# Kernel tuning notes

Measured on AMD Instinct MI355X. Metric: run time of the kernel, lower is better.

## Reference

```python
import jax, jax.numpy as jnp
import numpy as np
from jax import lax

B, T = 32, 512
CHAR_V, WORD_V, K = 120, 100000, 15
E = 128            # char/word embedding dim
D = 2 * E          # fusion dim = 256
H = 128            # hidden per direction (hidden_dim // 2)
L = 2              # num LSTM layers


def setup_inputs() -> dict:
    key = jax.random.key(0)
    ks = jax.random.split(key, 16)
    char_ids = jax.random.randint(ks[0], (B, T), 0, CHAR_V)
    word_ids = jax.random.randint(ks[1], (B, T), 0, WORD_V)
    tags = jax.random.randint(ks[2], (B, T), 0, K)
    mask = jnp.ones((B, T), dtype=bool)
    s = 0.1
    char_emb = jax.random.normal(ks[3], (CHAR_V, E), jnp.float32) * s
    char_emb = char_emb.at[0].set(0.0)  # padding_idx=0
    word_emb = jax.random.normal(ks[4], (WORD_V, E), jnp.float32) * s
    word_emb = word_emb.at[0].set(0.0)
    # Both layers have input dim D (layer0: fusion 256, layer1: bi-output 256),
    # so stack params as (layer, direction, ...). PyTorch gate order: i,f,g,o.
    lstm_wih = jax.random.normal(ks[5], (L, 2, 4 * H, D), jnp.float32) * s
    lstm_whh = jax.random.normal(ks[6], (L, 2, 4 * H, H), jnp.float32) * s
    lstm_bih = jax.random.normal(ks[7], (L, 2, 4 * H), jnp.float32) * s
    lstm_bhh = jax.random.normal(ks[8], (L, 2, 4 * H), jnp.float32) * s
    fc_w = jax.random.normal(ks[9], (K, 2 * H), jnp.float32) * s
    fc_b = jax.random.normal(ks[10], (K,), jnp.float32) * s
    trans = jax.random.normal(ks[11], (K, K), jnp.float32) * s
    start_trans = jax.random.normal(ks[12], (K,), jnp.float32) * s
    end_trans = jax.random.normal(ks[13], (K,), jnp.float32) * s
    return dict(char_ids=char_ids, word_ids=word_ids, tags=tags, mask=mask,
                char_emb=char_emb, word_emb=word_emb,
                lstm_wih=lstm_wih, lstm_whh=lstm_whh,
                lstm_bih=lstm_bih, lstm_bhh=lstm_bhh,
                fc_w=fc_w, fc_b=fc_b,
                trans=trans, start_trans=start_trans, end_trans=end_trans)


def _lstm_dir(xs, wih, whh, bih, bhh, reverse):
    # xs: (T, B, Din) -> hs: (T, B, H)
    pre = jnp.einsum('tbd,hd->tbh', xs, wih) + bih + bhh  # hoisted input GEMM
    h0 = jnp.zeros((xs.shape[1], whh.shape[1]), xs.dtype)
    def step(carry, p):
        h, c = carry
        g = p + h @ whh.T
        i, f, gg, o = jnp.split(g, 4, axis=-1)
        c = jax.nn.sigmoid(f) * c + jax.nn.sigmoid(i) * jnp.tanh(gg)
        h = jax.nn.sigmoid(o) * jnp.tanh(c)
        return (h, c), h
    _, hs = lax.scan(step, (h0, h0), pre, reverse=reverse)
    return hs


def _crf_nll(emissions, tags, maskf, trans, start, end):
    # emissions (T,B,K), tags (T,B) int, maskf (T,B) float. Returns -sum(logL).
    Tn, Bn, Kn = emissions.shape
    bidx = jnp.arange(Bn)
    # numerator: score of gold path
    num0 = start[tags[0]] + emissions[0, bidx, tags[0]]
    def nstep(s, inp):
        em_t, tg_t, tg_p, m_t = inp
        return s + (trans[tg_p, tg_t] + em_t[bidx, tg_t]) * m_t, None
    num, _ = lax.scan(nstep, num0, (emissions[1:], tags[1:], tags[:-1], maskf[1:]))
    seq_ends = maskf.sum(0).astype(jnp.int32) - 1
    num = num + end[tags[seq_ends, bidx]]
    # denominator: forward algorithm (logsumexp over all paths)
    alpha0 = start[None, :] + emissions[0]  # (B,K)
    def dstep(a, inp):
        em_t, m_t = inp
        nxt = jax.nn.logsumexp(a[:, :, None] + trans[None] + em_t[:, None, :], axis=1)
        return jnp.where(m_t[:, None] > 0, nxt, a), None
    alpha, _ = lax.scan(dstep, alpha0, (emissions[1:], maskf[1:]))
    den = jax.nn.logsumexp(alpha + end[None, :], axis=1)
    return -(num - den).sum()


def reference(char_ids, word_ids, tags, mask, char_emb, word_emb,
              lstm_wih, lstm_whh, lstm_bih, lstm_bhh,
              fc_w, fc_b, trans, start_trans, end_trans):
    fused = jnp.concatenate([char_emb[char_ids], word_emb[word_ids]], axis=-1)  # (B,T,256)
    xs = fused.transpose(1, 0, 2)  # (T,B,256)
    for l in range(L):  # dropout is identity in eval/deterministic reference
        hf = _lstm_dir(xs, lstm_wih[l, 0], lstm_whh[l, 0], lstm_bih[l, 0], lstm_bhh[l, 0], False)
        hb = _lstm_dir(xs, lstm_wih[l, 1], lstm_whh[l, 1], lstm_bih[l, 1], lstm_bhh[l, 1], True)
        xs = jnp.concatenate([hf, hb], axis=-1)  # (T,B,256)
    emissions = jnp.einsum('tbh,kh->tbk', xs, fc_w) + fc_b  # (T,B,15)
    maskf = mask.T.astype(emissions.dtype)
    return _crf_nll(emissions, tags.T, maskf, trans, start_trans, end_trans)
```

## Files before the change

kernel.cpp:

```cpp
#include <hip/hip_runtime.h>

#define TT 512
#define BB 32
#define KK 15
#define PGD 8

typedef __attribute__((ext_vector_type(8))) short short8;
typedef __attribute__((ext_vector_type(4))) float f32x4;
typedef __attribute__((ext_vector_type(8))) unsigned short us8;
typedef __attribute__((ext_vector_type(4))) unsigned short us4;
typedef __attribute__((ext_vector_type(2))) unsigned int u32x2;

__device__ __forceinline__ float bf2f(unsigned short u){
  union { unsigned int i; float f; } v; v.i = ((unsigned int)u) << 16; return v.f;
}
__device__ __forceinline__ unsigned short f2bf(float f){
  union { float f; unsigned int i; } v; v.f = f;
  return (unsigned short)((v.i + 0x7fffu + ((v.i >> 16) & 1u)) >> 16);
}
__device__ __forceinline__ float bflo(unsigned int u){ return __int_as_float((int)(u << 16)); }
__device__ __forceinline__ float bfhi(unsigned int u){ return __int_as_float((int)(u & 0xffff0000u)); }

__global__ void k_prep_embed(const float* __restrict__ wih, const float* __restrict__ whh,
                       const float* __restrict__ bih, const float* __restrict__ bhh,
                       const float* __restrict__ fcw,
                       unsigned short* __restrict__ wih_bf, unsigned short* __restrict__ whh_bf,
                       float* __restrict__ bias, unsigned short* __restrict__ fcw_bf,
                       const int* __restrict__ cid, const int* __restrict__ wid,
                       const float* __restrict__ cemb, const float* __restrict__ wemb,
                       unsigned short* __restrict__ x){
  int bx = blockIdx.x, tid = threadIdx.x;
  if (bx < 2048){
    int i = bx * 256 + tid;
    if (i < 2*2*512*256) wih_bf[i] = f2bf(wih[i]);
    if (i < 2*2*512*128) whh_bf[i] = f2bf(whh[i]);
    if (i < 2*2*512)     bias[i]   = bih[i] + bhh[i];
    if (i < 16*256)      fcw_bf[i] = (i < 15*256) ? f2bf(fcw[i]) : (unsigned short)0;
  } else {
    int m = (bx - 2048)*2 + (tid >> 7);
    int d = tid & 127;
    int t = m >> 5, b = m & 31;
    int c = cid[b*TT + t], w = wid[b*TT + t];
    x[(size_t)m*256 + d]       = f2bf(cemb[c*128 + d]);
    x[(size_t)m*256 + 128 + d] = f2bf(wemb[(size_t)w*128 + d]);
  }
}

__global__ __launch_bounds__(256) void k_gemm_pre(const unsigned short* __restrict__ x,
                        const unsigned short* __restrict__ wih_bf,
                        const float* __restrict__ bias,
                        unsigned short* __restrict__ pre){
  int lane = threadIdx.x & 63, wv = threadIdx.x >> 6;
  int m0 = blockIdx.x * 128 + wv * 32;
  int t = m0 >> 5;
  int by = blockIdx.y;
  int r16 = lane & 15, q4 = lane >> 4;
  const unsigned short* arow0 = x + (size_t)(m0 + r16)*256 + q4*8;
  const unsigned short* arow1 = arow0 + 16*256;
  short8 a0[8], a1[8];
  #pragma unroll
  for (int ks = 0; ks < 8; ++ks){ a0[ks] = *(const short8*)(arow0 + ks*32);
                                  a1[ks] = *(const short8*)(arow1 + ks*32); }
  f32x4 acc0[8], acc1[8];
  float bs[8];
  #pragma unroll
  for (int sub = 0; sub < 8; ++sub){
    int dir = sub >> 2, g = sub & 3;
    int n0 = dir*512 + g*128 + by*16;
    const unsigned short* brow = wih_bf + (size_t)(n0 + r16)*256 + q4*8;
    f32x4 z0 = {0.f,0.f,0.f,0.f}, z1 = {0.f,0.f,0.f,0.f};
    #pragma unroll
    for (int ks = 0; ks < 8; ++ks){
      short8 bfr = *(const short8*)(brow + ks*32);
      z0 = __builtin_amdgcn_mfma_f32_16x16x32_bf16(a0[ks], bfr, z0, 0, 0, 0);
      z1 = __builtin_amdgcn_mfma_f32_16x16x32_bf16(a1[ks], bfr, z1, 0, 0, 0);
    }
    acc0[sub] = z0; acc1[sub] = z1;
    bs[sub] = bias[n0 + r16];
  }
  #pragma unroll
  for (int dir = 0; dir < 2; ++dir){
    size_t pb0 = ((((size_t)dir*TT + t)*8 + q4)*8 + by)*256;
    size_t pb1 = ((((size_t)dir*TT + t)*8 + 4 + q4)*8 + by)*256;
    #pragma unroll
    for (int rr = 0; rr < 4; ++rr){
      us4 s0, s1;
      #pragma unroll
      for (int g = 0; g < 4; ++g){
        s0[g] = f2bf(acc0[dir*4+g][rr] + bs[dir*4+g]);
        s1[g] = f2bf(acc1[dir*4+g][rr] + bs[dir*4+g]);
      }
      *(us4*)(pre + pb0 + (size_t)((r16*4 + rr)*4)) = s0;
      *(us4*)(pre + pb1 + (size_t)((r16*4 + rr)*4)) = s1;
    }
  }
}

__global__ __launch_bounds__(512) void k_lstm(const unsigned short* __restrict__ pre,
                                              const unsigned short* __restrict__ whh_bf,
                                              unsigned short* __restrict__ y){
  const int dir = blockIdx.x >> 3, grp = blockIdx.x & 7;
  const int tid = threadIdx.x, lane = tid & 63, w = tid >> 6;
  const int r16 = lane & 15, q4 = lane >> 4;
  __shared__ __align__(16) unsigned char hbuf[2*1024];
  __shared__ __align__(16) unsigned char scratch[8*1024];
  *(unsigned int*)(hbuf + tid*4) = 0u;

  short8 afrag[4][4];
  const unsigned short* whhd = whh_bf + (size_t)dir*512*128;
  #pragma unroll
  for (int j = 0; j < 4; ++j){
    int wrow = (r16 & 3)*128 + w*16 + j*4 + (r16 >> 2);
    #pragma unroll
    for (int ks = 0; ks < 4; ++ks)
      afrag[j][ks] = *(const short8*)(whhd + (size_t)wrow*128 + ks*32 + q4*8);
  }

  const int t0 = dir ? TT-1 : 0;
  const ptrdiff_t ts = dir ? -16384 : 16384;
  const unsigned short* gbase = pre + ((((size_t)dir*TT + t0)*8 + grp)*8 + w)*256 + lane*4;
  u32x2 pgbuf[PGD];
  #pragma unroll
  for (int s = 0; s < PGD; ++s) pgbuf[s] = *(const u32x2*)(gbase + s*ts);
  const unsigned short* gptr = gbase + PGD*ts;

  const unsigned sw = (unsigned)(r16 << 5);
  const unsigned char* hb = hbuf + r16*256;
  const unsigned bo0 = (  0u + q4*16) ^ sw, bo1 = ( 64u + q4*16) ^ sw,
                 bo2 = (128u + q4*16) ^ sw, bo3 = (192u + q4*16) ^ sw;
  const unsigned scw_off = (unsigned)(size_t)(__attribute__((address_space(3))) unsigned char*)
                           (scratch + w*1024 + q4*32 + r16*8);
  const unsigned char* scr8 = scratch + w*1024 + (size_t)lane*8;
  const int hc = w*16 + (lane >> 2), bbn = lane & 3;
  unsigned char* hwp = hbuf + bbn*256 + (((unsigned)(hc*2)) ^ (bbn << 5));
  const bool act4 = (r16 < 4);
  const bool yw = (w < 4) && act4;
  const ptrdiff_t tsy = dir ? -(BB*256) : (BB*256);
  unsigned short* ysptr = y + ((size_t)t0*BB + grp*4 + r16)*256 + dir*128 + w*32 + q4*8 - tsy;
  const float L2E = 1.4426950408889634f;
  float cst = 0.f;
  short8 bf0 = {}, bf1 = {}, bf2 = {}, bf3 = {};

  __syncthreads();

  for (int it = 0; it < TT/PGD; ++it){
    #pragma unroll
    for (int bd = 0; bd < PGD; ++bd){
      const int p = bd & 1;
      if (act4){
        bf0 = *(const short8*)(hb + p*1024 + bo0);
        bf1 = *(const short8*)(hb + p*1024 + bo1);
        bf2 = *(const short8*)(hb + p*1024 + bo2);
        bf3 = *(const short8*)(hb + p*1024 + bo3);
      }
      f32x4 acc[4];
      #pragma unroll
      for (int j = 0; j < 4; ++j){
        f32x4 z = {0.f,0.f,0.f,0.f};
        z = __builtin_amdgcn_mfma_f32_16x16x32_bf16(afrag[j][0], bf0, z, 0, 0, 0);
        z = __builtin_amdgcn_mfma_f32_16x16x32_bf16(afrag[j][1], bf1, z, 0, 0, 0);
        z = __builtin_amdgcn_mfma_f32_16x16x32_bf16(afrag[j][2], bf2, z, 0, 0, 0);
        z = __builtin_amdgcn_mfma_f32_16x16x32_bf16(afrag[j][3], bf3, z, 0, 0, 0);
        acc[j] = z;
      }
      if ((it + bd) != 0 && yw){
        short8 hv = (w==0) ? bf0 : (w==1) ? bf1 : (w==2) ? bf2 : bf3;
        *(short8*)ysptr = hv;
      }
      ysptr += tsy;
      if (act4){
        u32x2 pk0, pk1, pk2, pk3;
        asm("v_cvt_pk_bf16_f32 %0, %1, %2" : "=v"(pk0.x) : "v"(acc[0][0]), "v"(acc[0][1]));
        asm("v_cvt_pk_bf16_f32 %0, %1, %2" : "=v"(pk0.y) : "v"(acc[0][2]), "v"(acc[0][3]));
        asm("v_cvt_pk_bf16_f32 %0, %1, %2" : "=v"(pk1.x) : "v"(acc[1][0]), "v"(acc[1][1]));
        asm("v_cvt_pk_bf16_f32 %0, %1, %2" : "=v"(pk1.y) : "v"(acc[1][2]), "v"(acc[1][3]));
        asm("v_cvt_pk_bf16_f32 %0, %1, %2" : "=v"(pk2.x) : "v"(acc[2][0]), "v"(acc[2][1]));
        asm("v_cvt_pk_bf16_f32 %0, %1, %2" : "=v"(pk2.y) : "v"(acc[2][2]), "v"(acc[2][3]));
        asm("v_cvt_pk_bf16_f32 %0, %1, %2" : "=v"(pk3.x) : "v"(acc[3][0]), "v"(acc[3][1]));
        asm("v_cvt_pk_bf16_f32 %0, %1, %2" : "=v"(pk3.y) : "v"(acc[3][2]), "v"(acc[3][3]));
        asm volatile("ds_write2_b64 %0, %1, %2 offset0:0 offset1:16"
                     :: "v"(scw_off), "v"(pk0), "v"(pk1) : "memory");
        asm volatile("ds_write2_b64 %0, %1, %2 offset0:32 offset1:48"
                     :: "v"(scw_off), "v"(pk2), "v"(pk3) : "memory");
      }
      u32x2 gvp = *(const u32x2*)scr8;
      u32x2 pgp = pgbuf[bd];
      pgbuf[bd] = *(const u32x2*)gptr;
      gptr += ts;
      float ai = bflo(gvp.x) + bflo(pgp.x);
      float af = bfhi(gvp.x) + bfhi(pgp.x);
      float ag = bflo(gvp.y) + bflo(pgp.y);
      float ao = bfhi(gvp.y) + bfhi(pgp.y);
      float si = __builtin_amdgcn_rcpf(1.f + __builtin_amdgcn_exp2f(-ai*L2E));
      float sf = __builtin_amdgcn_rcpf(1.f + __builtin_amdgcn_exp2f(-af*L2E));
      float tg = 1.f - 2.f*__builtin_amdgcn_rcpf(1.f + __builtin_amdgcn_exp2f(ag*(2.f*L2E)));
      float so = __builtin_amdgcn_rcpf(1.f + __builtin_amdgcn_exp2f(-ao*L2E));
      cst = sf*cst + si*tg;
      float th = 1.f - 2.f*__builtin_amdgcn_rcpf(1.f + __builtin_amdgcn_exp2f(cst*(2.f*L2E)));
      *(unsigned short*)(hwp + (p^1)*1024) = f2bf(so*th);
      asm volatile("s_waitcnt lgkmcnt(0)" ::: "memory");
      __builtin_amdgcn_s_barrier();
    }
  }
  if (yw){
    short8 hv = *(const short8*)(hb + ((w*64 + q4*16) ^ sw));
    *(short8*)ysptr = hv;
  }
}

__global__ __launch_bounds__(256) void k_emis(const unsigned short* __restrict__ y,
                       const unsigned short* __restrict__ fcw_bf,
                       const float* __restrict__ fcb, float* __restrict__ em){
  int lane = threadIdx.x & 63, wv = threadIdx.x >> 6;
  int r16 = lane & 15, q4 = lane >> 4;
  int m0 = blockIdx.x * 64 + wv * 16;
  const unsigned short* arow = y + (size_t)(m0 + r16)*256 + q4*8;
  const unsigned short* brow = fcw_bf + (size_t)r16*256 + q4*8;
  f32x4 acc = {0.f,0.f,0.f,0.f};
  #pragma unroll
  for (int ks = 0; ks < 8; ++ks){
    short8 a = *(const short8*)(arow + ks*32);
    short8 b = *(const short8*)(brow + ks*32);
    acc = __builtin_amdgcn_mfma_f32_16x16x32_bf16(a, b, acc, 0, 0, 0);
  }
  if (r16 < 15){
    float bs = fcb[r16];
    #pragma unroll
    for (int rr = 0; rr < 4; ++rr)
      em[(size_t)(m0 + q4*4 + rr)*16 + r16] = acc[rr] + bs;
  }
}

__global__ __launch_bounds__(64) void k_crf_den(const float* __restrict__ em,
                    const int* __restrict__ mask, const float* __restrict__ trans,
                    const float* __restrict__ startt, const float* __restrict__ endt,
                    float* __restrict__ dens){
  int lane = threadIdx.x & 63;
  int g = lane >> 4, j = lane & 15;
  int b = blockIdx.x*4 + g;
  int jj = j < 15 ? j : 14;
  const float L2E = 1.4426950408889634f, LN2 = 0.6931471805599453f;
  float tr_j[15];
  #pragma unroll
  for (int i = 0; i < 15; ++i) tr_j[i] = trans[i*15 + jj];
  float alpha = startt[jj] + em[b*16 + jj];
  int pbase = (lane & 48) << 2;
  auto body = [&](float em_t, int mk){
    float v[15];
    int ai = __float_as_int(alpha);
    #pragma unroll
    for (int i = 0; i < 15; ++i)
      v[i] = __int_as_float(__builtin_amdgcn_ds_bpermute(pbase + i*4, ai)) + tr_j[i];
    float mx = v[0];
    float e[15];
    #pragma unroll
    for (int i = 1; i < 15; ++i) e[i] = __builtin_amdgcn_exp2f((v[i]-mx)*L2E);
    float s = 1.f + ((e[1]+(e[2]+e[3])) + ((e[4]+e[5])+(e[6]+e[7])))
            + (((e[8]+e[9])+(e[10]+e[11])) + ((e[12]+e[13])+e[14]));
    float nxt = mx + __builtin_amdgcn_logf(s)*LN2 + em_t;
    alpha = mk ? nxt : alpha;
  };
  float emA = em[((size_t)1*BB + b)*16 + jj], emB = em[((size_t)2*BB + b)*16 + jj];
  int mkA = mask[b*TT + 1], mkB = mask[b*TT + 2];
  for (int t = 1; t + 1 < TT; t += 2){
    int ta = t+2 < TT ? t+2 : TT-1;
    int tb = t+3 < TT ? t+3 : TT-1;
    float emA2 = em[((size_t)ta*BB + b)*16 + jj];
    float emB2 = em[((size_t)tb*BB + b)*16 + jj];
    int mkA2 = mask[b*TT + ta], mkB2 = mask[b*TT + tb];
    body(emA, mkA);
    body(emB, mkB);
    emA = emA2; emB = emB2; mkA = mkA2; mkB = mkB2;
  }
  body(emA, mkA);
  float val = (j < 15) ? alpha + endt[j] : -3.0e38f;
  float mx = val;
  #pragma unroll
  for (int off = 8; off; off >>= 1) mx = fmaxf(mx, __shfl_xor(mx, off, 16));
  float ee = (j < 15) ? __builtin_amdgcn_exp2f((val-mx)*L2E) : 0.f;
  #pragma unroll
  for (int off = 8; off; off >>= 1) ee += __shfl_xor(ee, off, 16);
  if (j == 0) dens[b] = mx + __builtin_amdgcn_logf(ee)*LN2;
}

__global__ __launch_bounds__(512) void k_crf_fin(const float* __restrict__ em, const int* __restrict__ tags,
                    const int* __restrict__ mask, const float* __restrict__ trans,
                    const float* __restrict__ startt, const float* __restrict__ endt,
                    const float* __restrict__ dens, float* __restrict__ out){
  __shared__ float sh_tr[15][16];
  __shared__ float sh_s[16], sh_e[16];
  __shared__ float red[8];
  __shared__ int seqend[32];
  int tid = threadIdx.x, wv = tid >> 6;
  if (tid < 225) sh_tr[tid/15][tid%15] = trans[tid];
  if (tid < 15){ sh_s[tid] = startt[tid]; sh_e[tid] = endt[tid]; }
  {
    int b2 = tid >> 4, ch = tid & 15;
    int cnt = 0;
    #pragma unroll 4
    for (int t2 = 0; t2 < 32; ++t2) cnt += (mask[b2*TT + ch*32 + t2] != 0) ? 1 : 0;
    #pragma unroll
    for (int off = 8; off; off >>= 1) cnt += __shfl_down(cnt, off, 16);
    if (ch == 0) seqend[b2] = cnt - 1;
  }
  __syncthreads();
  float num = 0.f;
  #pragma unroll 4
  for (int i = tid; i < BB*TT; i += 512){
    int b2 = i >> 9, t = i & (TT-1);
    int tg = tags[b2*TT + t];
    if (t == 0){
      num += sh_s[tg] + em[b2*16 + tg];
    } else if (mask[b2*TT + t] != 0){
      int tp = tags[b2*TT + t - 1];
      num += sh_tr[tp][tg] + em[((size_t)t*BB + b2)*16 + tg];
    }
  }
  if (tid < 32) num += sh_e[tags[tid*TT + seqend[tid]]];
  #pragma unroll
  for (int off = 32; off; off >>= 1) num += __shfl_down(num, off, 64);
  if ((tid & 63) == 0) red[wv] = num;
  __syncthreads();
  if (tid == 0){
    float numtot = 0.f;
    #pragma unroll
    for (int i = 0; i < 8; ++i) numtot += red[i];
    float dentot = 0.f;
    for (int i = 0; i < 32; ++i) dentot += dens[i];
    out[0] = dentot - numtot;
  }
}

extern "C" void kernel_launch(void* const* d_in, const int* in_sizes, int n_in,
                              void* d_out, int out_size, void* d_ws, size_t ws_size,
                              hipStream_t stream){
  const int*   cid  = (const int*)d_in[0];
  const int*   wid  = (const int*)d_in[1];
  const int*   tags = (const int*)d_in[2];
  const int*   mask = (const int*)d_in[3];
  const float* cemb = (const float*)d_in[4];
  const float* wemb = (const float*)d_in[5];
  const float* wih  = (const float*)d_in[6];
  const float* whh  = (const float*)d_in[7];
  const float* bih  = (const float*)d_in[8];
  const float* bhh  = (const float*)d_in[9];
  const float* fcw  = (const float*)d_in[10];
  const float* fcb  = (const float*)d_in[11];
  const float* trans= (const float*)d_in[12];
  const float* st   = (const float*)d_in[13];
  const float* en   = (const float*)d_in[14];

  char* ws = (char*)d_ws;
  size_t off = 0;
  auto alloc = [&](size_t bytes){ size_t o = off; off += (bytes + 255) & ~(size_t)255; return o; };
  unsigned short* wih_bf = (unsigned short*)(ws + alloc((size_t)2*2*512*256*2));
  unsigned short* whh_bf = (unsigned short*)(ws + alloc((size_t)2*2*512*128*2));
  float*          bias   = (float*)         (ws + alloc((size_t)2*2*512*4));
  unsigned short* fcw_bf = (unsigned short*)(ws + alloc((size_t)16*256*2));
  unsigned short* x0     = (unsigned short*)(ws + alloc((size_t)TT*BB*256*2));
  unsigned short* x1     = (unsigned short*)(ws + alloc((size_t)TT*BB*256*2));
  unsigned short* pre    = (unsigned short*)(ws + alloc((size_t)2*TT*BB*512*2));
  float*          em     = (float*)         (ws + alloc((size_t)TT*BB*16*4));
  float*          dens   = (float*)         (ws + alloc((size_t)32*4));

  k_prep_embed<<<2048 + TT*BB/2, 256, 0, stream>>>(wih, whh, bih, bhh, fcw,
                                                   wih_bf, whh_bf, bias, fcw_bf,
                                                   cid, wid, cemb, wemb, x0);
  for (int l = 0; l < 2; ++l){
    const unsigned short* xin = l ? x1 : x0;
    unsigned short* yout = l ? x0 : x1;
    k_gemm_pre<<<dim3(128,8), 256, 0, stream>>>(xin, wih_bf + (size_t)l*2*512*256,
                                                bias + (size_t)l*1024, pre);
    k_lstm<<<16, 512, 0, stream>>>(pre, whh_bf + (size_t)l*2*512*128, yout);
  }
  k_emis<<<256, 256, 0, stream>>>(x0, fcw_bf, fcb, em);
  k_crf_den<<<8, 64, 0, stream>>>(em, mask, trans, st, en, dens);
  k_crf_fin<<<1, 512, 0, stream>>>(em, tags, mask, trans, st, en, dens, (float*)d_out);
}
```

Before: 866.3 us.

## Halve LSTM block to 4 waves, each computing 32 hidden columns

The recurrent LSTM kernel now runs 4 waves of 256 threads instead of 8 waves, with each wave holding twice the recurrent weight fragments and computing two hidden units per lane. This cuts the number of waves that take part in the per-step barrier and shared-memory handoff, which sits on the serial critical path of the 512-step recurrence. In exchange each wave issues twice the MFMAs and gate math per step and uses more registers, which could lengthen each step.

Measured after the change: 1.095 ms. 26.4% more time.

```diff
diff --git a/kernel.cpp b/kernel.cpp
--- a/kernel.cpp
+++ b/kernel.cpp
@@ -96,21 +96,21 @@
   }
 }
 
-__global__ __launch_bounds__(512) void k_lstm(const unsigned short* __restrict__ pre,
+__global__ __launch_bounds__(256) void k_lstm(const unsigned short* __restrict__ pre,
                                               const unsigned short* __restrict__ whh_bf,
                                               unsigned short* __restrict__ y){
   const int dir = blockIdx.x >> 3, grp = blockIdx.x & 7;
   const int tid = threadIdx.x, lane = tid & 63, w = tid >> 6;
   const int r16 = lane & 15, q4 = lane >> 4;
   __shared__ __align__(16) unsigned char hbuf[2*1024];
-  __shared__ __align__(16) unsigned char scratch[8*1024];
-  *(unsigned int*)(hbuf + tid*4) = 0u;
-
-  short8 afrag[4][4];
+  __shared__ __align__(16) unsigned char scratch[4*2048];
+  *(unsigned long long*)(hbuf + tid*8) = 0ull;
+
+  short8 afrag[8][4];
   const unsigned short* whhd = whh_bf + (size_t)dir*512*128;
   #pragma unroll
-  for (int j = 0; j < 4; ++j){
-    int wrow = (r16 & 3)*128 + w*16 + j*4 + (r16 >> 2);
+  for (int j = 0; j < 8; ++j){
+    int wrow = (r16 & 3)*128 + w*32 + j*4 + (r16 >> 2);
     #pragma unroll
     for (int ks = 0; ks < 4; ++ks)
       afrag[j][ks] = *(const short8*)(whhd + (size_t)wrow*128 + ks*32 + q4*8);
@@ -118,10 +118,13 @@
 
   const int t0 = dir ? TT-1 : 0;
   const ptrdiff_t ts = dir ? -16384 : 16384;
-  const unsigned short* gbase = pre + ((((size_t)dir*TT + t0)*8 + grp)*8 + w)*256 + lane*4;
-  u32x2 pgbuf[PGD];
-  #pragma unroll
-  for (int s = 0; s < PGD; ++s) pgbuf[s] = *(const u32x2*)(gbase + s*ts);
+  const unsigned short* gbase = pre + ((((size_t)dir*TT + t0)*8 + grp)*8 + w*2)*256 + lane*4;
+  u32x2 pgA[PGD], pgB[PGD];
+  #pragma unroll
+  for (int s = 0; s < PGD; ++s){
+    pgA[s] = *(const u32x2*)(gbase + s*ts);
+    pgB[s] = *(const u32x2*)(gbase + 256 + s*ts);
+  }
   const unsigned short* gptr = gbase + PGD*ts;
 
   const unsigned sw = (unsigned)(r16 << 5);
@@ -129,16 +132,16 @@
   const unsigned bo0 = (  0u + q4*16) ^ sw, bo1 = ( 64u + q4*16) ^ sw,
                  bo2 = (128u + q4*16) ^ sw, bo3 = (192u + q4*16) ^ sw;
   const unsigned scw_off = (unsigned)(size_t)(__attribute__((address_space(3))) unsigned char*)
-                           (scratch + w*1024 + q4*32 + r16*8);
-  const unsigned char* scr8 = scratch + w*1024 + (size_t)lane*8;
-  const int hc = w*16 + (lane >> 2), bbn = lane & 3;
-  unsigned char* hwp = hbuf + bbn*256 + (((unsigned)(hc*2)) ^ (bbn << 5));
+                           (scratch + w*2048 + q4*32 + r16*8);
+  const unsigned char* scr8 = scratch + w*2048 + q4*128 + ((r16 >> 2))*32 + (r16 & 3)*8;
+  const int hc0 = w*32 + (lane >> 2), bbn = lane & 3;
+  unsigned char* hwp0 = hbuf + bbn*256 + (((unsigned)(hc0*2)) ^ (bbn << 5));
+  unsigned char* hwp1 = hbuf + bbn*256 + (((unsigned)((hc0+16)*2)) ^ (bbn << 5));
   const bool act4 = (r16 < 4);
-  const bool yw = (w < 4) && act4;
   const ptrdiff_t tsy = dir ? -(BB*256) : (BB*256);
   unsigned short* ysptr = y + ((size_t)t0*BB + grp*4 + r16)*256 + dir*128 + w*32 + q4*8 - tsy;
   const float L2E = 1.4426950408889634f;
-  float cst = 0.f;
+  float cst0 = 0.f, cst1 = 0.f;
   short8 bf0 = {}, bf1 = {}, bf2 = {}, bf3 = {};
 
   __syncthreads();
@@ -153,9 +156,9 @@
         bf2 = *(const short8*)(hb + p*1024 + bo2);
         bf3 = *(const short8*)(hb + p*1024 + bo3);
       }
-      f32x4 acc[4];
+      f32x4 acc[8];
       #pragma unroll
-      for (int j = 0; j < 4; ++j){
+      for (int j = 0; j < 8; ++j){
         f32x4 z = {0.f,0.f,0.f,0.f};
         z = __builtin_amdgcn_mfma_f32_16x16x32_bf16(afrag[j][0], bf0, z, 0, 0, 0);
         z = __builtin_amdgcn_mfma_f32_16x16x32_bf16(afrag[j][1], bf1, z, 0, 0, 0);
@@ -163,46 +166,65 @@
         z = __builtin_amdgcn_mfma_f32_16x16x32_bf16(afrag[j][3], bf3, z, 0, 0, 0);
         acc[j] = z;
       }
-      if ((it + bd) != 0 && yw){
+      if ((it + bd) != 0 && act4){
         short8 hv = (w==0) ? bf0 : (w==1) ? bf1 : (w==2) ? bf2 : bf3;
         *(short8*)ysptr = hv;
       }
       ysptr += tsy;
       if (act4){
-        u32x2 pk0, pk1, pk2, pk3;
-        asm("v_cvt_pk_bf16_f32 %0, %1, %2" : "=v"(pk0.x) : "v"(acc[0][0]), "v"(acc[0][1]));
-        asm("v_cvt_pk_bf16_f32 %0, %1, %2" : "=v"(pk0.y) : "v"(acc[0][2]), "v"(acc[0][3]));
-        asm("v_cvt_pk_bf16_f32 %0, %1, %2" : "=v"(pk1.x) : "v"(acc[1][0]), "v"(acc[1][1]));
-        asm("v_cvt_pk_bf16_f32 %0, %1, %2" : "=v"(pk1.y) : "v"(acc[1][2]), "v"(acc[1][3]));
-        asm("v_cvt_pk_bf16_f32 %0, %1, %2" : "=v"(pk2.x) : "v"(acc[2][0]), "v"(acc[2][1]));
-        asm("v_cvt_pk_bf16_f32 %0, %1, %2" : "=v"(pk2.y) : "v"(acc[2][2]), "v"(acc[2][3]));
-        asm("v_cvt_pk_bf16_f32 %0, %1, %2" : "=v"(pk3.x) : "v"(acc[3][0]), "v"(acc[3][1]));
-        asm("v_cvt_pk_bf16_f32 %0, %1, %2" : "=v"(pk3.y) : "v"(acc[3][2]), "v"(acc[3][3]));
+        u32x2 pk[8];
+        #pragma unroll
+        for (int j = 0; j < 8; ++j){
+          asm("v_cvt_pk_bf16_f32 %0, %1, %2" : "=v"(pk[j].x) : "v"(acc[j][0]), "v"(acc[j][1]));
+          asm("v_cvt_pk_bf16_f32 %0, %1, %2" : "=v"(pk[j].y) : "v"(acc[j][2]), "v"(acc[j][3]));
+        }
         asm volatile("ds_write2_b64 %0, %1, %2 offset0:0 offset1:16"
-                     :: "v"(scw_off), "v"(pk0), "v"(pk1) : "memory");
+                     :: "v"(scw_off), "v"(pk[0]), "v"(pk[1]) : "memory");
         asm volatile("ds_write2_b64 %0, %1, %2 offset0:32 offset1:48"
-                     :: "v"(scw_off), "v"(pk2), "v"(pk3) : "memory");
-      }
-      u32x2 gvp = *(const u32x2*)scr8;
-      u32x2 pgp = pgbuf[bd];
-      pgbuf[bd] = *(const u32x2*)gptr;
+                     :: "v"(scw_off), "v"(pk[2]), "v"(pk[3]) : "memory");
+        asm volatile("ds_write2_b64 %0, %1, %2 offset0:64 offset1:80"
+                     :: "v"(scw_off), "v"(pk[4]), "v"(pk[5]) : "memory");
+        asm volatile("ds_write2_b64 %0, %1, %2 offset0:96 offset1:112"
+                     :: "v"(scw_off), "v"(pk[6]), "v"(pk[7]) : "memory");
+      }
+      u32x2 gv0 = *(const u32x2*)scr8;
+      u32x2 gv1 = *(const u32x2*)(scr8 + 512);
+      u32x2 pga = pgA[bd];
+      u32x2 pgb = pgB[bd];
+      pgA[bd] = *(const u32x2*)gptr;
+      pgB[bd] = *(const u32x2*)(gptr + 256);
       gptr += ts;
-      float ai = bflo(gvp.x) + bflo(pgp.x);
-      float af = bfhi(gvp.x) + bfhi(pgp.x);
-      float ag = bflo(gvp.y) + bflo(pgp.y);
-      float ao = bfhi(gvp.y) + bfhi(pgp.y);
-      float si = __builtin_amdgcn_rcpf(1.f + __builtin_amdgcn_exp2f(-ai*L2E));
-      float sf = __builtin_amdgcn_rcpf(1.f + __builtin_amdgcn_exp2f(-af*L2E));
-      float tg = 1.f - 2.f*__builtin_amdgcn_rcpf(1.f + __builtin_amdgcn_exp2f(ag*(2.f*L2E)));
-      float so = __builtin_amdgcn_rcpf(1.f + __builtin_amdgcn_exp2f(-ao*L2E));
-      cst = sf*cst + si*tg;
-      float th = 1.f - 2.f*__builtin_amdgcn_rcpf(1.f + __builtin_amdgcn_exp2f(cst*(2.f*L2E)));
-      *(unsigned short*)(hwp + (p^1)*1024) = f2bf(so*th);
+      {
+        float ai = bflo(gv0.x) + bflo(pga.x);
+        float af = bfhi(gv0.x) + bfhi(pga.x);
+        float ag = bflo(gv0.y) + bflo(pga.y);
+        float ao = bfhi(gv0.y) + bfhi(pga.y);
+        float si = __builtin_amdgcn_rcpf(1.f + __builtin_amdgcn_exp2f(-ai*L2E));
+        float sf = __builtin_amdgcn_rcpf(1.f + __builtin_amdgcn_exp2f(-af*L2E));
+        float tg = 1.f - 2.f*__builtin_amdgcn_rcpf(1.f + __builtin_amdgcn_exp2f(ag*(2.f*L2E)));
+        float so = __builtin_amdgcn_rcpf(1.f + __builtin_amdgcn_exp2f(-ao*L2E));
+        cst0 = sf*cst0 + si*tg;
+        float th = 1.f - 2.f*__builtin_amdgcn_rcpf(1.f + __builtin_amdgcn_exp2f(cst0*(2.f*L2E)));
+        *(unsigned short*)(hwp0 + (p^1)*1024) = f2bf(so*th);
+      }
+      {
+        float ai = bflo(gv1.x) + bflo(pgb.x);
+        float af = bfhi(gv1.x) + bfhi(pgb.x);
+        float ag = bflo(gv1.y) + bflo(pgb.y);
+        float ao = bfhi(gv1.y) + bfhi(pgb.y);
+        float si = __builtin_amdgcn_rcpf(1.f + __builtin_amdgcn_exp2f(-ai*L2E));
+        float sf = __builtin_amdgcn_rcpf(1.f + __builtin_amdgcn_exp2f(-af*L2E));
+        float tg = 1.f - 2.f*__builtin_amdgcn_rcpf(1.f + __builtin_amdgcn_exp2f(ag*(2.f*L2E)));
+        float so = __builtin_amdgcn_rcpf(1.f + __builtin_amdgcn_exp2f(-ao*L2E));
+        cst1 = sf*cst1 + si*tg;
+        float th = 1.f - 2.f*__builtin_amdgcn_rcpf(1.f + __builtin_amdgcn_exp2f(cst1*(2.f*L2E)));
+        *(unsigned short*)(hwp1 + (p^1)*1024) = f2bf(so*th);
+      }
       asm volatile("s_waitcnt lgkmcnt(0)" ::: "memory");
       __builtin_amdgcn_s_barrier();
     }
   }
-  if (yw){
+  if (act4){
     short8 hv = *(const short8*)(hb + ((w*64 + q4*16) ^ sw));
     *(short8*)ysptr = hv;
   }
@@ -371,7 +393,7 @@
     unsigned short* yout = l ? x0 : x1;
     k_gemm_pre<<<dim3(128,8), 256, 0, stream>>>(xin, wih_bf + (size_t)l*2*512*256,
                                                 bias + (size_t)l*1024, pre);
-    k_lstm<<<16, 512, 0, stream>>>(pre, whh_bf + (size_t)l*2*512*128, yout);
+    k_lstm<<<16, 256, 0, stream>>>(pre, whh_bf + (size_t)l*2*512*128, yout);
   }
   k_emis<<<256, 256, 0, stream>>>(x0, fcw_bf, fcb, em);
   k_crf_den<<<8, 64, 0, stream>>>(em, mask, trans, st, en, dens);
```

## Process two batch groups per LSTM block, halving the grid

Applied to the files above, without the earlier changes.

Each recurrent LSTM block now handles two 4-sample batch groups, issuing two interleaved MFMA chains per gate tile with one shared barrier per time step. Weight fragments held in registers are reused across both groups and the block count drops from 16 to 8. This aims to amortise the per-step sync and latency overhead, at the cost of doubling per-step MFMA and activation work and LDS usage on the serial critical path.

Result: slower. 1.411 ms (+62.9%).

```diff
diff --git a/kernel.cpp b/kernel.cpp
--- a/kernel.cpp
+++ b/kernel.cpp
@@ -20,6 +20,21 @@
 }
 __device__ __forceinline__ float bflo(unsigned int u){ return __int_as_float((int)(u << 16)); }
 __device__ __forceinline__ float bfhi(unsigned int u){ return __int_as_float((int)(u & 0xffff0000u)); }
+
+__device__ __forceinline__ unsigned short lstm_act(u32x2 gvp, u32x2 pgp, float& cst){
+  const float L2E = 1.4426950408889634f;
+  float ai = bflo(gvp.x) + bflo(pgp.x);
+  float af = bfhi(gvp.x) + bfhi(pgp.x);
+  float ag = bflo(gvp.y) + bflo(pgp.y);
+  float ao = bfhi(gvp.y) + bfhi(pgp.y);
+  float si = __builtin_amdgcn_rcpf(1.f + __builtin_amdgcn_exp2f(-ai*L2E));
+  float sf = __builtin_amdgcn_rcpf(1.f + __builtin_amdgcn_exp2f(-af*L2E));
+  float tg = 1.f - 2.f*__builtin_amdgcn_rcpf(1.f + __builtin_amdgcn_exp2f(ag*(2.f*L2E)));
+  float so = __builtin_amdgcn_rcpf(1.f + __builtin_amdgcn_exp2f(-ao*L2E));
+  cst = sf*cst + si*tg;
+  float th = 1.f - 2.f*__builtin_amdgcn_rcpf(1.f + __builtin_amdgcn_exp2f(cst*(2.f*L2E)));
+  return f2bf(so*th);
+}
 
 __global__ void k_prep_embed(const float* __restrict__ wih, const float* __restrict__ whh,
                        const float* __restrict__ bih, const float* __restrict__ bhh,
@@ -99,12 +114,13 @@
 __global__ __launch_bounds__(512) void k_lstm(const unsigned short* __restrict__ pre,
                                               const unsigned short* __restrict__ whh_bf,
                                               unsigned short* __restrict__ y){
-  const int dir = blockIdx.x >> 3, grp = blockIdx.x & 7;
+  const int dir = blockIdx.x >> 2, bp = blockIdx.x & 3;
+  const int gA = bp*2, gB = gA + 1;
   const int tid = threadIdx.x, lane = tid & 63, w = tid >> 6;
   const int r16 = lane & 15, q4 = lane >> 4;
-  __shared__ __align__(16) unsigned char hbuf[2*1024];
-  __shared__ __align__(16) unsigned char scratch[8*1024];
-  *(unsigned int*)(hbuf + tid*4) = 0u;
+  __shared__ __align__(16) unsigned char hbuf[4096];
+  __shared__ __align__(16) unsigned char scratch[16384];
+  *(unsigned long long*)(hbuf + tid*8) = 0ull;
 
   short8 afrag[4][4];
   const unsigned short* whhd = whh_bf + (size_t)dir*512*128;
@@ -118,28 +134,33 @@
 
   const int t0 = dir ? TT-1 : 0;
   const ptrdiff_t ts = dir ? -16384 : 16384;
-  const unsigned short* gbase = pre + ((((size_t)dir*TT + t0)*8 + grp)*8 + w)*256 + lane*4;
-  u32x2 pgbuf[PGD];
-  #pragma unroll
-  for (int s = 0; s < PGD; ++s) pgbuf[s] = *(const u32x2*)(gbase + s*ts);
-  const unsigned short* gptr = gbase + PGD*ts;
+  const unsigned short* gbaseA = pre + ((((size_t)dir*TT + t0)*8 + gA)*8 + w)*256 + lane*4;
+  u32x2 pgA[PGD], pgB[PGD];
+  #pragma unroll
+  for (int s = 0; s < PGD; ++s){
+    pgA[s] = *(const u32x2*)(gbaseA + s*ts);
+    pgB[s] = *(const u32x2*)(gbaseA + 2048 + s*ts);
+  }
+  const unsigned short* gptr = gbaseA + PGD*ts;
 
   const unsigned sw = (unsigned)(r16 << 5);
-  const unsigned char* hb = hbuf + r16*256;
+  const unsigned char* hbA = hbuf + r16*256;
   const unsigned bo0 = (  0u + q4*16) ^ sw, bo1 = ( 64u + q4*16) ^ sw,
                  bo2 = (128u + q4*16) ^ sw, bo3 = (192u + q4*16) ^ sw;
-  const unsigned scw_off = (unsigned)(size_t)(__attribute__((address_space(3))) unsigned char*)
-                           (scratch + w*1024 + q4*32 + r16*8);
-  const unsigned char* scr8 = scratch + w*1024 + (size_t)lane*8;
+  const unsigned scwA_off = (unsigned)(size_t)(__attribute__((address_space(3))) unsigned char*)
+                            (scratch + w*1024 + q4*32 + r16*8);
+  const unsigned scwB_off = scwA_off + 8192;
+  const unsigned char* scrA = scratch + w*1024 + (size_t)lane*8;
   const int hc = w*16 + (lane >> 2), bbn = lane & 3;
-  unsigned char* hwp = hbuf + bbn*256 + (((unsigned)(hc*2)) ^ (bbn << 5));
+  unsigned char* hwpA = hbuf + bbn*256 + (((unsigned)(hc*2)) ^ (bbn << 5));
   const bool act4 = (r16 < 4);
-  const bool yw = (w < 4) && act4;
+  const int ws4 = w & 3;
   const ptrdiff_t tsy = dir ? -(BB*256) : (BB*256);
-  unsigned short* ysptr = y + ((size_t)t0*BB + grp*4 + r16)*256 + dir*128 + w*32 + q4*8 - tsy;
-  const float L2E = 1.4426950408889634f;
-  float cst = 0.f;
-  short8 bf0 = {}, bf1 = {}, bf2 = {}, bf3 = {};
+  unsigned short* ysptr = y + ((size_t)t0*BB + (w < 4 ? gA : gB)*4 + r16)*256
+                            + dir*128 + ws4*32 + q4*8 - tsy;
+  float cstA = 0.f, cstB = 0.f;
+  short8 bfA0 = {}, bfA1 = {}, bfA2 = {}, bfA3 = {};
+  short8 bfB0 = {}, bfB1 = {}, bfB2 = {}, bfB3 = {};
 
   __syncthreads();
 
@@ -148,62 +169,80 @@
     for (int bd = 0; bd < PGD; ++bd){
       const int p = bd & 1;
       if (act4){
-        bf0 = *(const short8*)(hb + p*1024 + bo0);
-        bf1 = *(const short8*)(hb + p*1024 + bo1);
-        bf2 = *(const short8*)(hb + p*1024 + bo2);
-        bf3 = *(const short8*)(hb + p*1024 + bo3);
+        bfA0 = *(const short8*)(hbA + p*1024 + bo0);
+        bfA1 = *(const short8*)(hbA + p*1024 + bo1);
+        bfA2 = *(const short8*)(hbA + p*1024 + bo2);
+        bfA3 = *(const short8*)(hbA + p*1024 + bo3);
+        bfB0 = *(const short8*)(hbA + 2048 + p*1024 + bo0);
+        bfB1 = *(const short8*)(hbA + 2048 + p*1024 + bo1);
+        bfB2 = *(const short8*)(hbA + 2048 + p*1024 + bo2);
+        bfB3 = *(const short8*)(hbA + 2048 + p*1024 + bo3);
       }
-      f32x4 acc[4];
+      f32x4 accA[4], accB[4];
       #pragma unroll
       for (int j = 0; j < 4; ++j){
-        f32x4 z = {0.f,0.f,0.f,0.f};
-        z = __builtin_amdgcn_mfma_f32_16x16x32_bf16(afrag[j][0], bf0, z, 0, 0, 0);
-        z = __builtin_amdgcn_mfma_f32_16x16x32_bf16(afrag[j][1], bf1, z, 0, 0, 0);
-        z = __builtin_amdgcn_mfma_f32_16x16x32_bf16(afrag[j][2], bf2, z, 0, 0, 0);
-        z = __builtin_amdgcn_mfma_f32_16x16x32_bf16(afrag[j][3], bf3, z, 0, 0, 0);
-        acc[j] = z;
+        f32x4 za = {0.f,0.f,0.f,0.f}, zb = {0.f,0.f,0.f,0.f};
+        za = __builtin_amdgcn_mfma_f32_16x16x32_bf16(afrag[j][0], bfA0, za, 0, 0, 0);
+        za = __builtin_amdgcn_mfma_f32_16x16x32_bf16(afrag[j][1], bfA1, za, 0, 0, 0);
+        za = __builtin_amdgcn_mfma_f32_16x16x32_bf16(afrag[j][2], bfA2, za, 0, 0, 0);
+        za = __builtin_amdgcn_mfma_f32_16x16x32_bf16(afrag[j][3], bfA3, za, 0, 0, 0);
+        zb = __builtin_amdgcn_mfma_f32_16x16x32_bf16(afrag[j][0], bfB0, zb, 0, 0, 0);
+        zb = __builtin_amdgcn_mfma_f32_16x16x32_bf16(afrag[j][1], bfB1, zb, 0, 0, 0);
+        zb = __builtin_amdgcn_mfma_f32_16x16x32_bf16(afrag[j][2], bfB2, zb, 0, 0, 0);
+        zb = __builtin_amdgcn_mfma_f32_16x16x32_bf16(afrag[j][3], bfB3, zb, 0, 0, 0);
+        accA[j] = za; accB[j] = zb;
       }
-      if ((it + bd) != 0 && yw){
-        short8 hv = (w==0) ? bf0 : (w==1) ? bf1 : (w==2) ? bf2 : bf3;
+      if ((it + bd) != 0 && act4){
+        short8 hv;
+        if (w < 4) hv = (ws4==0) ? bfA0 : (ws4==1) ? bfA1 : (ws4==2) ? bfA2 : bfA3;
+        else       hv = (ws4==0) ? bfB0 : (ws4==1) ? bfB1 : (ws4==2) ? bfB2 : bfB3;
         *(short8*)ysptr = hv;
       }
       ysptr += tsy;
       if (act4){
-        u32x2 pk0, pk1, pk2, pk3;
-        asm("v_cvt_pk_bf16_f32 %0, %1, %2" : "=v"(pk0.x) : "v"(acc[0][0]), "v"(acc[0][1]));
-        asm("v_cvt_pk_bf16_f32 %0, %1, %2" : "=v"(pk0.y) : "v"(acc[0][2]), "v"(acc[0][3]));
-        asm("v_cvt_pk_bf16_f32 %0, %1, %2" : "=v"(pk1.x) : "v"(acc[1][0]), "v"(acc[1][1]));
-        asm("v_cvt_pk_bf16_f32 %0, %1, %2" : "=v"(pk1.y) : "v"(acc[1][2]), "v"(acc[1][3]));
-        asm("v_cvt_pk_bf16_f32 %0, %1, %2" : "=v"(pk2.x) : "v"(acc[2][0]), "v"(acc[2][1]));
-        asm("v_cvt_pk_bf16_f32 %0, %1, %2" : "=v"(pk2.y) : "v"(acc[2][2]), "v"(acc[2][3]));
-        asm("v_cvt_pk_bf16_f32 %0, %1, %2" : "=v"(pk3.x) : "v"(acc[3][0]), "v"(acc[3][1]));
-        asm("v_cvt_pk_bf16_f32 %0, %1, %2" : "=v"(pk3.y) : "v"(acc[3][2]), "v"(acc[3][3]));
+        u32x2 pa0, pa1, pa2, pa3, pb0, pb1, pb2, pb3;
+        asm("v_cvt_pk_bf16_f32 %0, %1, %2" : "=v"(pa0.x) : "v"(accA[0][0]), "v"(accA[0][1]));
+        asm("v_cvt_pk_bf16_f32 %0, %1, %2" : "=v"(pa0.y) : "v"(accA[0][2]), "v"(accA[0][3]));
+        asm("v_cvt_pk_bf16_f32 %0, %1, %2" : "=v"(pa1.x) : "v"(accA[1][0]), "v"(accA[1][1]));
+        asm("v_cvt_pk_bf16_f32 %0, %1, %2" : "=v"(pa1.y) : "v"(accA[1][2]), "v"(accA[1][3]));
+        asm("v_cvt_pk_bf16_f32 %0, %1, %2" : "=v"(pa2.x) : "v"(accA[2][0]), "v"(accA[2][1]));
+        asm("v_cvt_pk_bf16_f32 %0, %1, %2" : "=v"(pa2.y) : "v"(accA[2][2]), "v"(accA[2][3]));
+        asm("v_cvt_pk_bf16_f32 %0, %1, %2" : "=v"(pa3.x) : "v"(accA[3][0]), "v"(accA[3][1]));
+        asm("v_cvt_pk_bf16_f32 %0, %1, %2" : "=v"(pa3.y) : "v"(accA[3][2]), "v"(accA[3][3]));
+        asm("v_cvt_pk_bf16_f32 %0, %1, %2" : "=v"(pb0.x) : "v"(accB[0][0]), "v"(accB[0][1]));
+        asm("v_cvt_pk_bf16_f32 %0, %1, %2" : "=v"(pb0.y) : "v"(accB[0][2]), "v"(accB[0][3]));
+        asm("v_cvt_pk_bf16_f32 %0, %1, %2" : "=v"(pb1.x) : "v"(accB[1][0]), "v"(accB[1][1]));
+        asm("v_cvt_pk_bf16_f32 %0, %1, %2" : "=v"(pb1.y) : "v"(accB[1][2]), "v"(accB[1][3]));
+        asm("v_cvt_pk_bf16_f32 %0, %1, %2" : "=v"(pb2.x) : "v"(accB[2][0]), "v"(accB[2][1]));
+        asm("v_cvt_pk_bf16_f32 %0, %1, %2" : "=v"(pb2.y) : "v"(accB[2][2]), "v"(accB[2][3]));
+        asm("v_cvt_pk_bf16_f32 %0, %1, %2" : "=v"(pb3.x) : "v"(accB[3][0]), "v"(accB[3][1]));
+        asm("v_cvt_pk_bf16_f32 %0, %1, %2" : "=v"(pb3.y) : "v"(accB[3][2]), "v"(accB[3][3]));
         asm volatile("ds_write2_b64 %0, %1, %2 offset0:0 offset1:16"
-                     :: "v"(scw_off), "v"(pk0), "v"(pk1) : "memory");
+                     :: "v"(scwA_off), "v"(pa0), "v"(pa1) : "memory");
         asm volatile("ds_write2_b64 %0, %1, %2 offset0:32 offset1:48"
-                     :: "v"(scw_off), "v"(pk2), "v"(pk3) : "memory");
+                     :: "v"(scwA_off), "v"(pa2), "v"(pa3) : "memory");
+        asm volatile("ds_write2_b64 %0, %1, %2 offset0:0 offset1:16"
+                     :: "v"(scwB_off), "v"(pb0), "v"(pb1) : "memory");
+        asm volatile("ds_write2_b64 %0, %1, %2 offset0:32 offset1:48"
+                     :: "v"(scwB_off), "v"(pb2), "v"(pb3) : "memory");
       }
-      u32x2 gvp = *(const u32x2*)scr8;
-      u32x2 pgp = pgbuf[bd];
-      pgbuf[bd] = *(const u32x2*)gptr;
+      u32x2 gvA = *(const u32x2*)scrA;
+      u32x2 gvB = *(const u32x2*)(scrA + 8192);
+      u32x2 pga = pgA[bd], pgb = pgB[bd];
+      pgA[bd] = *(const u32x2*)gptr;
+      pgB[bd] = *(const u32x2*)(gptr + 2048);
       gptr += ts;
-      float ai = bflo(gvp.x) + bflo(pgp.x);
-      float af = bfhi(gvp.x) + bfhi(pgp.x);
-      float ag = bflo(gvp.y) + bflo(pgp.y);
-      float ao = bfhi(gvp.y) + bfhi(pgp.y);
-      float si = __builtin_amdgcn_rcpf(1.f + __builtin_amdgcn_exp2f(-ai*L2E));
-      float sf = __builtin_amdgcn_rcpf(1.f + __builtin_amdgcn_exp2f(-af*L2E));
-      float tg = 1.f - 2.f*__builtin_amdgcn_rcpf(1.f + __builtin_amdgcn_exp2f(ag*(2.f*L2E)));
-      float so = __builtin_amdgcn_rcpf(1.f + __builtin_amdgcn_exp2f(-ao*L2E));
-      cst = sf*cst + si*tg;
-      float th = 1.f - 2.f*__builtin_amdgcn_rcpf(1.f + __builtin_amdgcn_exp2f(cst*(2.f*L2E)));
-      *(unsigned short*)(hwp + (p^1)*1024) = f2bf(so*th);
+      unsigned short hA = lstm_act(gvA, pga, cstA);
+      unsigned short hB = lstm_act(gvB, pgb, cstB);
+      *(unsigned short*)(hwpA + (p^1)*1024) = hA;
+      *(unsigned short*)(hwpA + 2048 + (p^1)*1024) = hB;
       asm volatile("s_waitcnt lgkmcnt(0)" ::: "memory");
       __builtin_amdgcn_s_barrier();
     }
   }
-  if (yw){
-    short8 hv = *(const short8*)(hb + ((w*64 + q4*16) ^ sw));
+  if (act4){
+    const unsigned char* hbT = (w < 4) ? hbA : (hbA + 2048);
+    short8 hv = *(const short8*)(hbT + ((ws4*64 + q4*16) ^ sw));
     *(short8*)ysptr = hv;
   }
 }
@@ -371,7 +410,7 @@
     unsigned short* yout = l ? x0 : x1;
     k_gemm_pre<<<dim3(128,8), 256, 0, stream>>>(xin, wih_bf + (size_t)l*2*512*256,
                                                 bias + (size_t)l*1024, pre);
-    k_lstm<<<16, 512, 0, stream>>>(pre, whh_bf + (size_t)l*2*512*128, yout);
+    k_lstm<<<8, 512, 0, stream>>>(pre, whh_bf + (size_t)l*2*512*128, yout);
   }
   k_emis<<<256, 256, 0, stream>>>(x0, fcw_bf, fcb, em);
   k_crf_den<<<8, 64, 0, stream>>>(em, mask, trans, st, en, dens);
```
